# Kernel tuning notes

Measured on AMD Instinct MI355X. Metric: run time of the kernel, lower is better.

Reference implementation:

```python
import jax, jax.numpy as jnp
import numpy as np
from math import sqrt

B, T_IN, N = 32, 12, 512
C = 32                 # d_model (residual == dilation channels)
SKIP_CH, END_CH = 256, 512
OUT_DIM = 12
NHEADS, CH1 = 4, 32    # graph generator heads / per-head dim
L = 8                  # blocks(4) * layers(2)
DILATIONS = [1, 2, 1, 2, 1, 2, 1, 2]
RF = 13                # receptive field = 1 + 4*(2^2 - 1)
KS = [10, 20, 40, 500]
EPS = 1e-5


def conv1x1(x, w, b):
    # x: (B,Cin,N,T), w: (Cout,Cin)
    return jnp.einsum('bcnt,oc->bont', x, w) + b[None, :, None, None]


def dconv(x, w, b, d):
    # dilated temporal conv, kernel (1,2): w (Cout,Cin,2); out T' = T - d
    Tc = x.shape[-1]
    y = (jnp.einsum('bcnt,oc->bont', x[..., :Tc - d], w[:, :, 0])
         + jnp.einsum('bcnt,oc->bont', x[..., d:], w[:, :, 1]))
    return y + b[None, :, None, None]


def gcn_apply(x, A, w, b, batched):
    # x (B,c,N,T); A (S,N,N) static or (B,S,N,N) dynamic; out channels = mlp((S+1)*c)
    Bb, c, n, t = x.shape
    sub = 'bcvt,bsvw->bscwt' if batched else 'bcvt,svw->bscwt'
    x1 = jnp.einsum(sub, x, A).reshape(Bb, -1, n, t)
    return conv1x1(jnp.concatenate([x, x1], axis=1), w, b)


def setup_inputs() -> dict:
    key = jax.random.key(0)
    ks = iter(jax.random.split(key, 64))
    def nrm(shape, fan):
        return jax.random.normal(next(ks), shape, jnp.float32) / np.float32(sqrt(fan))
    inp = {}
    inp['input'] = jax.random.normal(next(ks), (B, T_IN, N), jnp.float32)
    inp['supports'] = jax.random.uniform(next(ks), (2, N, N), jnp.float32) / np.float32(N)
    inp['emb'] = jax.random.normal(next(ks), (1, N, 12), jnp.float32)
    inp['embds_w'] = nrm((12, 1), 12); inp['embds_b'] = jnp.zeros((1,), jnp.float32)
    inp['wl_w'] = nrm((12, CH1 * NHEADS), 12); inp['wl_b'] = jnp.zeros((CH1 * NHEADS,), jnp.float32)
    inp['wr_w'] = nrm((12, CH1 * NHEADS), 12); inp['wr_b'] = jnp.zeros((CH1 * NHEADS,), jnp.float32)
    inp['start_w'] = nrm((C, 1), 1); inp['start_b'] = jnp.zeros((C,), jnp.float32)
    inp['filter_w'] = nrm((L, C, C, 2), 2 * C); inp['filter_b'] = jnp.zeros((L, C), jnp.float32)
    inp['gate_w'] = nrm((L, C, C, 2), 2 * C); inp['gate_b'] = jnp.zeros((L, C), jnp.float32)
    inp['skip_w'] = nrm((L, SKIP_CH, C), C); inp['skip_b'] = jnp.zeros((L, SKIP_CH), jnp.float32)
    inp['bn_g'] = jnp.ones((L, C), jnp.float32); inp['bn_b'] = jnp.zeros((L, C), jnp.float32)
    inp['gconv_w'] = nrm((L, C, 5 * C), 5 * C); inp['gconv_b'] = jnp.zeros((L, C), jnp.float32)
    inp['dyn_w'] = nrm((L, C, 5 * C), 5 * C); inp['dyn_b'] = jnp.zeros((L, C), jnp.float32)
    inp['end1_w'] = nrm((END_CH, SKIP_CH), SKIP_CH); inp['end1_b'] = jnp.zeros((END_CH,), jnp.float32)
    inp['end2_w'] = nrm((OUT_DIM, END_CH), END_CH); inp['end2_b'] = jnp.zeros((OUT_DIM,), jnp.float32)
    return inp


def reference(input, supports, emb, embds_w, embds_b, wl_w, wl_b, wr_w, wr_b,
              start_w, start_b, filter_w, filter_b, gate_w, gate_b,
              skip_w, skip_b, bn_g, bn_b, gconv_w, gconv_b, dyn_w, dyn_b,
              end1_w, end1_b, end2_w, end2_b):
    x_in = jnp.transpose(input, (0, 2, 1))[:, None]           # (B,1,N,12)
    # Embedding: project time dim to 1, add learned node embedding (broadcast back to 12)
    g = (x_in @ embds_w + embds_b) + emb                      # (B,1,N,12)
    feature = g[:, 0]                                         # (B,N,12)
    # multi-head attention scores -> dynamic adjacency candidates
    l = (feature @ wl_w + wl_b).reshape(B, N, NHEADS, CH1).transpose(0, 2, 1, 3)
    r = (feature @ wr_w + wr_b).reshape(B, N, NHEADS, CH1).transpose(0, 2, 1, 3)
    att = jnp.einsum('bhnd,bhmd->bhnm', l, r) / np.float32(sqrt(CH1))   # (B,4,N,N)
    # per-head top-k sparsify (scatter into -1e20) then row softmax
    bi = jnp.arange(B)[:, None, None]
    ri = jnp.arange(N)[None, :, None]
    heads = []
    for h in range(NHEADS):
        a = att[:, h]
        kv, ki = jax.lax.top_k(a, min(KS[h], N))
        m = jnp.full((B, N, N), -1e20, a.dtype).at[bi, ri, ki].set(kv)
        heads.append(jax.nn.softmax(m, axis=-1))
    dyn = jnp.stack(heads, axis=1)                            # (B,4,N,N)
    # static supports: [a0, a0@a0, a1, a1@a1]
    s0, s1 = supports[0], supports[1]
    sup = jnp.stack([s0, s0 @ s0, s1, s1 @ s1], axis=0)        # (4,N,N)
    # left-pad time to receptive field
    x = jnp.pad(x_in, ((0, 0), (0, 0), (0, 0), (RF - T_IN, 0)))
    x = conv1x1(x, start_w, start_b)                          # (B,C,N,13)
    skip = None
    for i, d in enumerate(DILATIONS):
        residual = x
        x = jnp.tanh(dconv(x, filter_w[i], filter_b[i], d)) * jax.nn.sigmoid(dconv(x, gate_w[i], gate_b[i], d))
        s = conv1x1(x, skip_w[i], skip_b[i])
        skip = s if skip is None else s + skip[..., -s.shape[-1]:]
        x = gcn_apply(x, dyn, dyn_w[i], dyn_b[i], True)
        x = gcn_apply(x, sup, gconv_w[i], gconv_b[i], False)
        x = x + residual[..., -x.shape[-1]:]
        # BatchNorm2d in eval mode (running_mean=0, running_var=1)
        x = x / np.float32(sqrt(1.0 + EPS)) * bn_g[i][None, :, None, None] + bn_b[i][None, :, None, None]
    x = jax.nn.relu(skip)                                     # (B,SKIP_CH,N,1)
    x = jax.nn.relu(conv1x1(x, end1_w, end1_b))
    x = conv1x1(x, end2_w, end2_b)                            # (B,12,N,1)
    return x[..., 0]                                          # (B,12,N)
```

## Files before the change

kernel.cpp:

```cpp
#include <hip/hip_runtime.h>
#include <math.h>

#define BB 32
#define NNODE 512
#define TIN 12
#define CCH 32
#define NH 4
#define DDIM 32
#define NL 8
#define SKC 256
#define ENDC 512
#define ODIM 12
#define RFP 13

typedef __attribute__((ext_vector_type(8))) short bf16x8;
typedef __attribute__((ext_vector_type(4))) float f32x4;

__device__ __forceinline__ float sigmoidf_(float x){ return 1.0f/(1.0f+expf(-x)); }
__device__ __forceinline__ unsigned short f2bf(float f){
  unsigned u = __float_as_uint(f);
  u += 0x7FFFu + ((u >> 16) & 1u);
  return (unsigned short)(u >> 16);
}
__device__ __forceinline__ float bf2f(unsigned short h){
  return __uint_as_float(((unsigned)h) << 16);
}
__device__ __forceinline__ void gload16(const void* g, void* l){
  __builtin_amdgcn_global_load_lds(
      (const __attribute__((address_space(1))) void*)g,
      (__attribute__((address_space(3))) void*)l, 16, 0, 0);
}

__global__ void k_feat_lr(const float* __restrict__ input, const float* __restrict__ emb,
                          const float* __restrict__ embds_w, const float* __restrict__ embds_b,
                          const float* __restrict__ wl_w, const float* __restrict__ wl_b,
                          const float* __restrict__ wr_w, const float* __restrict__ wr_b,
                          float* __restrict__ lbuf, float* __restrict__ rbuf){
  int bn = blockIdx.x;
  int b = bn >> 9, n = bn & 511;
  int j = threadIdx.x;
  __shared__ float f[TIN];
  if (j < TIN){
    float s = 0.f;
    for (int t = 0; t < TIN; ++t) s += input[(b*TIN + t)*NNODE + n] * embds_w[t];
    f[j] = s + embds_b[0] + emb[n*TIN + j];
  }
  __syncthreads();
  float lv = wl_b[j], rv = wr_b[j];
  for (int t = 0; t < TIN; ++t){
    float ft = f[t];
    lv += ft * wl_w[t*128 + j];
    rv += ft * wr_w[t*128 + j];
  }
  int h = j >> 5, d = j & 31;
  int o = ((b*NH + h)*NNODE + n)*DDIM + d;
  lbuf[o] = lv; rbuf[o] = rv;
}

__global__ __launch_bounds__(256) void k_att(const float* __restrict__ lbuf,
                      const float* __restrict__ rbuf, float* __restrict__ att){
  int bh = blockIdx.z;
  int n0 = blockIdx.y * 32, m0 = blockIdx.x * 32;
  int tid = threadIdx.x;
  int tx = tid & 31, ty = tid >> 5;
  __shared__ float Ls[32][33], Rs[32][33];
  const float* lb = lbuf + (size_t)bh*NNODE*DDIM;
  const float* rb = rbuf + (size_t)bh*NNODE*DDIM;
  for (int i = tid; i < 1024; i += 256){
    int r = i >> 5, c = i & 31;
    Ls[r][c] = lb[(n0+r)*DDIM + c];
    Rs[r][c] = rb[(m0+r)*DDIM + c];
  }
  __syncthreads();
  float acc[4] = {0.f,0.f,0.f,0.f};
  for (int d = 0; d < 32; ++d){
    float rv = Rs[tx][d];
    #pragma unroll
    for (int j = 0; j < 4; ++j) acc[j] += Ls[ty + 8*j][d] * rv;
  }
  #pragma unroll
  for (int j = 0; j < 4; ++j)
    att[((size_t)bh*NNODE + n0+ty+8*j)*NNODE + m0 + tx] = acc[j] / sqrtf(32.0f);
}

__global__ __launch_bounds__(256) void k_topk_softmax(float* __restrict__ att){
  __shared__ int hist[4*256];
  int tid = threadIdx.x;
  int wid = tid >> 6, lane = tid & 63;
  int row = blockIdx.x*4 + wid;
  int h = (row >> 9) & 3;
  int k = (h==0)?10:(h==1)?20:(h==2)?40:500;
  float* rp = att + (size_t)row * NNODE;
  int* hh = hist + wid*256;
  float v[8]; unsigned a[8];
  #pragma unroll
  for (int j = 0; j < 8; ++j){
    v[j] = rp[j*64 + lane];
    unsigned u = __float_as_uint(v[j]);
    a[j] = (u & 0x80000000u) ? ~u : (u | 0x80000000u);
  }
  float m = v[0];
  #pragma unroll
  for (int j = 1; j < 8; ++j) m = fmaxf(m, v[j]);
  for (int off = 32; off; off >>= 1) m = fmaxf(m, __shfl_down(m, off, 64));
  float mx = __shfl(m, 0, 64);
  unsigned pfx = 0u; int kr = k;
  for (int rnd = 0; rnd < 4; ++rnd){
    int sh = 24 - rnd*8;
    #pragma unroll
    for (int i = 0; i < 4; ++i) hh[lane*4+i] = 0;
    __builtin_amdgcn_wave_barrier();
    #pragma unroll
    for (int j = 0; j < 8; ++j){
      bool c = (rnd == 0) || ((a[j] >> (sh+8)) == (pfx >> (sh+8)));
      if (c) atomicAdd(&hh[(a[j] >> sh) & 255], 1);
    }
    __builtin_amdgcn_wave_barrier();
    asm volatile("s_waitcnt lgkmcnt(0)" ::: "memory");
    int h0 = hh[lane*4], h1 = hh[lane*4+1], h2 = hh[lane*4+2], h3 = hh[lane*4+3];
    int s3 = h3, s2 = h2+s3, s1 = h1+s2, s0 = h0+s1;
    int t = s0;
    #pragma unroll
    for (int off = 1; off < 64; off <<= 1){
      int y = __shfl_down(t, off, 64);
      if (lane + off < 64) t += y;
    }
    int Asuf = __shfl_down(t, 1, 64);
    if (lane == 63) Asuf = 0;
    int cs0 = s0+Asuf, cs1 = s1+Asuf, cs2 = s2+Asuf, cs3 = s3+Asuf;
    int found = 0, dloc = 0, krloc = 0;
    if (cs0 >= kr && cs0-h0 < kr){ found=1; dloc=lane*4+0; krloc = kr-(cs0-h0); }
    if (cs1 >= kr && cs1-h1 < kr){ found=1; dloc=lane*4+1; krloc = kr-(cs1-h1); }
    if (cs2 >= kr && cs2-h2 < kr){ found=1; dloc=lane*4+2; krloc = kr-(cs2-h2); }
    if (cs3 >= kr && cs3-h3 < kr){ found=1; dloc=lane*4+3; krloc = kr-(cs3-h3); }
    unsigned long long msk = __ballot(found);
    int src = __ffsll((unsigned long long)msk) - 1;
    int db = __shfl(dloc, src, 64);
    kr = __shfl(krloc, src, 64);
    pfx = pfx | ((unsigned)db << sh);
  }
  unsigned uth = pfx; int neq = kr;
  unsigned long long em[8];
  #pragma unroll
  for (int j = 0; j < 8; ++j) em[j] = __ballot(a[j] == uth);
  int pcum[8]; int run = 0;
  #pragma unroll
  for (int j = 0; j < 8; ++j){ pcum[j] = run; run += (int)__popcll(em[j]); }
  unsigned long long below = (1ull << lane) - 1ull;
  float e[8]; float ssum = 0.f;
  #pragma unroll
  for (int j = 0; j < 8; ++j){
    bool kp = a[j] > uth;
    if (!kp && a[j] == uth){
      int rank = pcum[j] + (int)__popcll(em[j] & below);
      kp = rank < neq;
    }
    e[j] = kp ? expf(v[j] - mx) : 0.f;
    ssum += e[j];
  }
  for (int off = 32; off; off >>= 1) ssum += __shfl_down(ssum, off, 64);
  float tot = __shfl(ssum, 0, 64);
  unsigned short* rp16 = (unsigned short*)rp;
  #pragma unroll
  for (int j = 0; j < 8; ++j) rp16[j*64 + lane] = f2bf(e[j] / tot);
}

__global__ __launch_bounds__(256) void k_transpose_dyn(const unsigned short* __restrict__ dynBf,
                                                       unsigned short* __restrict__ dynT){
  int bs = blockIdx.z;
  int v0 = blockIdx.x*64, w0 = blockIdx.y*64;
  __shared__ unsigned short Ts[64][66];
  const unsigned short* S = dynBf + (size_t)bs*NNODE*1024;
  unsigned short* D = dynT + (size_t)bs*NNODE*NNODE;
  int tid = threadIdx.x;
  for (int i = tid; i < 4096; i += 256){
    int r = i >> 6, c = i & 63;
    Ts[r][c] = S[(size_t)(v0+r)*1024 + w0 + c];
  }
  __syncthreads();
  for (int i = tid; i < 4096; i += 256){
    int r = i >> 6, c = i & 63;
    D[(size_t)(w0+r)*NNODE + v0 + c] = Ts[c][r];
  }
}

__global__ __launch_bounds__(256) void k_supT_copy(const float* __restrict__ supports,
                                                   unsigned short* __restrict__ supT){
  int w = blockIdx.z;
  int v0 = blockIdx.x*64, n0 = blockIdx.y*64;
  __shared__ float Ts[64][65];
  const float* S = supports + (size_t)w*NNODE*NNODE;
  int tid = threadIdx.x;
  for (int i = tid; i < 4096; i += 256){
    int r = i >> 6, c = i & 63;
    Ts[r][c] = S[(size_t)(v0+r)*NNODE + n0 + c];
  }
  __syncthreads();
  for (int i = tid; i < 4096; i += 256){
    int r = i >> 6, c = i & 63;
    supT[((size_t)(2*w)*NNODE + n0 + r)*NNODE + v0 + c] = f2bf(Ts[c][r]);
  }
}

__global__ __launch_bounds__(256) void k_supT_sq(const float* __restrict__ supports,
                                                 unsigned short* __restrict__ supT){
  int which = blockIdx.z;
  const float* A = supports + (size_t)which*NNODE*NNODE;
  int w0 = blockIdx.x * 32, v0 = blockIdx.y * 32;
  int tid = threadIdx.x;
  int tx = tid & 31, tyg = tid >> 5;
  __shared__ float As[32][33], Bs[32][33], Cs[32][33];
  float acc[4] = {0.f,0.f,0.f,0.f};
  for (int k0 = 0; k0 < NNODE; k0 += 32){
    int lc = tid >> 3, lu0 = (tid & 7) * 4;
    __syncthreads();
    for (int u = 0; u < 4; ++u){
      As[lc][lu0+u] = A[(size_t)(v0+lc)*NNODE + k0 + lu0 + u];
      Bs[lc][lu0+u] = A[(size_t)(k0+lc)*NNODE + w0 + lu0 + u];
    }
    __syncthreads();
    for (int u = 0; u < 32; ++u){
      float bw = Bs[u][tx];
      #pragma unroll
      for (int j = 0; j < 4; ++j) acc[j] += As[tyg + 8*j][u] * bw;
    }
  }
  __syncthreads();
  #pragma unroll
  for (int j = 0; j < 4; ++j) Cs[tyg + 8*j][tx] = acc[j];
  __syncthreads();
  for (int i = tid; i < 1024; i += 256){
    int wl = i >> 5, vl = i & 31;
    supT[((size_t)(2*which+1)*NNODE + w0 + wl)*NNODE + v0 + vl] = f2bf(Cs[vl][wl]);
  }
}

__global__ void k_make_x0(const float* __restrict__ input, const float* __restrict__ start_w,
                          const float* __restrict__ start_b, float* __restrict__ x0){
  int idx = blockIdx.x*256 + threadIdx.x;
  const int total = BB*RFP*CCH*NNODE;
  if (idx >= total) return;
  int n = idx & 511;
  int rest = idx >> 9;
  int c = rest & 31; rest >>= 5;
  int t = rest % RFP;
  int b = rest / RFP;
  float v = (t == 0) ? 0.f : input[((size_t)b*TIN + (t-1))*NNODE + n];
  x0[idx] = start_w[c] * v + start_b[c];
}

__global__ __launch_bounds__(256) void k_dconv_act(const float* __restrict__ x,
      const float* __restrict__ fw, const float* __restrict__ fb,
      const float* __restrict__ gw, const float* __restrict__ gb,
      unsigned short* __restrict__ out,
      const float* __restrict__ sw, const float* __restrict__ sb,
      float* __restrict__ skip,
      int Tin, int Tp, int dil, int skipInit){
  int n0 = blockIdx.x * 64;
  int t = blockIdx.y;
  int b = blockIdx.z;
  int tid = threadIdx.x;
  int lane = tid & 63, cg = tid >> 6;
  __shared__ float X0[32][64], X1[32][64];
  __shared__ float fwl[32][32][2], gwl[32][32][2];
  __shared__ float gs[32][64];
  const float* xb0 = x + ((size_t)(b*Tin + t)*CCH)*NNODE;
  const float* xb1 = x + ((size_t)(b*Tin + t + dil)*CCH)*NNODE;
  for (int i = tid; i < 32*64; i += 256){
    int c = i >> 6, nn2 = i & 63;
    X0[c][nn2] = xb0[c*NNODE + n0 + nn2];
    X1[c][nn2] = xb1[c*NNODE + n0 + nn2];
  }
  for (int i = tid; i < 2048; i += 256){
    ((float*)fwl)[i] = fw[i];
    ((float*)gwl)[i] = gw[i];
  }
  __syncthreads();
  float F[8], G[8];
  #pragma unroll
  for (int j = 0; j < 8; ++j){ int c = cg*8 + j; F[j] = fb[c]; G[j] = gb[c]; }
  for (int cp = 0; cp < 32; ++cp){
    float x0v = X0[cp][lane], x1v = X1[cp][lane];
    #pragma unroll
    for (int j = 0; j < 8; ++j){
      int c = cg*8 + j;
      F[j] += x0v * fwl[c][cp][0] + x1v * fwl[c][cp][1];
      G[j] += x0v * gwl[c][cp][0] + x1v * gwl[c][cp][1];
    }
  }
  unsigned short* ob = out + ((size_t)(b*Tp + t)*CCH)*NNODE;
  #pragma unroll
  for (int j = 0; j < 8; ++j){
    int c = cg*8 + j;
    float gv = tanhf(F[j]) * sigmoidf_(G[j]);
    gs[c][lane] = gv;
    ob[c*NNODE + n0 + lane] = f2bf(gv);
  }
  if (t == Tp - 1){
    __syncthreads();
    float* skb = skip + ((size_t)b*SKC)*NNODE + n0 + lane;
    for (int er = 0; er < 64; ++er){
      int e = cg*64 + er;
      float acc2 = sb[e];
      #pragma unroll
      for (int c = 0; c < 32; ++c) acc2 += sw[e*32 + c] * gs[c][lane];
      float* dst = skb + (size_t)e*NNODE;
      *dst = skipInit ? acc2 : (*dst + acc2);
    }
  }
}

__global__ __launch_bounds__(256) void k_gcn_gemm(
    const unsigned short* __restrict__ A, const unsigned short* __restrict__ BT,
    const float* __restrict__ w, const float* __restrict__ bias,
    unsigned short* __restrict__ outBf, float* __restrict__ outF,
    const float* __restrict__ res, const float* __restrict__ bng,
    const float* __restrict__ bnb, int Tp, int dil, long long bStride){
  __shared__ short smem[16384 + 5376];
  short* AsL = smem;
  short* BsL = smem + 8192;
  short* Wc  = smem + 16384;
  short* Tt  = smem;
  int tid = threadIdx.x;
  int b = blockIdx.z;
  int n032 = blockIdx.x * 32;
  int t0 = blockIdx.y * 4;
  int Mb = Tp * 32;
  int rowBase = b*Mb + blockIdx.y*128;
  const unsigned short* Bb = BT + (size_t)b * bStride;
  int wid = tid >> 6, lane = tid & 63;
  int wm = wid >> 1, wn = wid & 1;
  int l15 = lane & 15, l4 = lane >> 4;
  for (int i = tid; i < 5120; i += 256){
    int o = i / 160, kk = i - o*160;
    Wc[o*168 + kk] = (short)f2bf(w[o*160 + ((kk < 128) ? (32 + kk) : (kk - 128))]);
  }
  f32x4 acc[4][4];
  #pragma unroll
  for (int mf = 0; mf < 4; ++mf)
    #pragma unroll
    for (int nf = 0; nf < 4; ++nf)
      acc[mf][nf] = (f32x4){0.f, 0.f, 0.f, 0.f};
  for (int k0 = 0; k0 < 512; k0 += 64){
    __syncthreads();
    #pragma unroll
    for (int it = 0; it < 4; ++it){
      int r = it*32 + (tid>>3), g = tid & 7;
      gload16(A + (size_t)(rowBase + r)*512 + k0 + ((g ^ (r&7))<<3), AsL + r*64 + (g<<3));
      int s = r >> 5, nl = r & 31;
      gload16(Bb + (size_t)((s<<9) + n032 + nl)*512 + k0 + ((g ^ (r&7))<<3), BsL + r*64 + (g<<3));
    }
    __syncthreads();
    #pragma unroll
    for (int ks = 0; ks < 2; ++ks){
      bf16x8 af[4], bfr[4];
      #pragma unroll
      for (int mf = 0; mf < 4; ++mf){
        int rr = wm*64 + mf*16 + l15;
        af[mf] = *(const bf16x8*)(AsL + rr*64 + (((ks*4 + l4) ^ (rr & 7)) << 3));
      }
      #pragma unroll
      for (int nf = 0; nf < 4; ++nf){
        int rr = wn*64 + nf*16 + l15;
        bfr[nf] = *(const bf16x8*)(BsL + rr*64 + (((ks*4 + l4) ^ (rr & 7)) << 3));
      }
      #pragma unroll
      for (int mf = 0; mf < 4; ++mf)
        #pragma unroll
        for (int nf = 0; nf < 4; ++nf)
          acc[mf][nf] = __builtin_amdgcn_mfma_f32_16x16x32_bf16(af[mf], bfr[nf], acc[mf][nf], 0, 0, 0);
    }
  }
  const float inv = 1.0f / sqrtf(1.0f + 1e-5f);
  for (int t = 0; t < 4; ++t){
    __syncthreads();
    if (wm == (t >> 1)){
      #pragma unroll
      for (int mf2 = 0; mf2 < 2; ++mf2){
        int mf = (t & 1)*2 + mf2;
        #pragma unroll
        for (int nf = 0; nf < 4; ++nf){
          int c128 = wn*64 + nf*16 + l15;
          int s = c128 >> 5, nl = c128 & 31;
          #pragma unroll
          for (int r = 0; r < 4; ++r){
            int cROW = mf2*16 + l4*4 + r;
            Tt[nl*168 + s*32 + cROW] = (short)f2bf(acc[mf][nf][r]);
          }
        }
      }
    }
    for (int i = tid; i < 1024; i += 256){
      int c = i >> 5, nl = i & 31;
      Tt[nl*168 + 128 + c] =
        (short)A[(size_t)(b*Mb + (t0+t)*32 + c)*512 + n032 + nl];
    }
    __syncthreads();
    f32x4 am = (f32x4){0.f,0.f,0.f,0.f};
    #pragma unroll
    for (int ks = 0; ks < 5; ++ks){
      bf16x8 af = *(const bf16x8*)(Wc + (wm*16 + l15)*168 + ks*32 + l4*8);
      bf16x8 bf = *(const bf16x8*)(Tt + (wn*16 + l15)*168 + ks*32 + l4*8);
      am = __builtin_amdgcn_mfma_f32_16x16x32_bf16(af, bf, am, 0, 0, 0);
    }
    if (t0 + t < Tp){
      int btG = b*Tp + t0 + t;
      #pragma unroll
      for (int r = 0; r < 4; ++r){
        int o = wm*16 + l4*4 + r;
        int nl = wn*16 + l15;
        size_t oidx = (size_t)(btG*32 + o)*512 + n032 + nl;
        float val = am[r] + bias[o];
        if (outBf){
          outBf[oidx] = f2bf(val);
        } else {
          float resv = res[(size_t)((b*(Tp+dil) + t0 + t + dil)*32 + o)*512 + n032 + nl];
          outF[oidx] = (val + resv) * (bng[o]*inv) + bnb[o];
        }
      }
    }
  }
}

__global__ __launch_bounds__(256) void k_gemm(
    const unsigned short* __restrict__ A, const unsigned short* __restrict__ BT,
    unsigned short* __restrict__ Y, int Mb, long long bStride,
    int K, int Ystride, int relu){
  __shared__ short As[128][64];
  __shared__ short Bs[128][64];
  int tid = threadIdx.x;
  int n0 = blockIdx.x * 128;
  int rowBase = blockIdx.z * Mb + blockIdx.y * 128;
  int rowEnd  = blockIdx.z * Mb + Mb;
  const unsigned short* Bb = BT + (size_t)blockIdx.z * bStride;
  int wid = tid >> 6, lane = tid & 63;
  int wm = wid >> 1, wn = wid & 1;
  int l15 = lane & 15, l4 = lane >> 4;
  f32x4 acc[4][4];
  #pragma unroll
  for (int mf = 0; mf < 4; ++mf)
    #pragma unroll
    for (int nf = 0; nf < 4; ++nf)
      acc[mf][nf] = (f32x4){0.f, 0.f, 0.f, 0.f};
  for (int k0 = 0; k0 < K; k0 += 64){
    __syncthreads();
    #pragma unroll
    for (int it = 0; it < 4; ++it){
      int r = it*32 + (tid>>3), g = tid & 7;
      gload16(A + (size_t)(rowBase + r)*K + k0 + ((g ^ (r&7))<<3), &As[r][g<<3]);
      gload16(Bb + (size_t)(n0 + r)*K + k0 + ((g ^ (r&7))<<3), &Bs[r][g<<3]);
    }
    __syncthreads();
    #pragma unroll
    for (int ks = 0; ks < 2; ++ks){
      bf16x8 af[4], bfr[4];
      #pragma unroll
      for (int mf = 0; mf < 4; ++mf){
        int r = wm*64 + mf*16 + l15;
        af[mf] = *(const bf16x8*)&As[r][(((ks*4 + l4) ^ (r & 7)) << 3)];
      }
      #pragma unroll
      for (int nf = 0; nf < 4; ++nf){
        int r = wn*64 + nf*16 + l15;
        bfr[nf] = *(const bf16x8*)&Bs[r][(((ks*4 + l4) ^ (r & 7)) << 3)];
      }
      #pragma unroll
      for (int mf = 0; mf < 4; ++mf)
        #pragma unroll
        for (int nf = 0; nf < 4; ++nf)
          acc[mf][nf] = __builtin_amdgcn_mfma_f32_16x16x32_bf16(af[mf], bfr[nf], acc[mf][nf], 0, 0, 0);
    }
  }
  #pragma unroll
  for (int mf = 0; mf < 4; ++mf){
    #pragma unroll
    for (int nf = 0; nf < 4; ++nf){
      #pragma unroll
      for (int r = 0; r < 4; ++r){
        int row = rowBase + wm*64 + mf*16 + l4*4 + r;
        if (row < rowEnd){
          int col = n0 + wn*64 + nf*16 + l15;
          float v = acc[mf][nf][r];
          if (relu) v = v > 0.f ? v : 0.f;
          Y[(size_t)row*Ystride + col] = f2bf(v);
        }
      }
    }
  }
}

__global__ __launch_bounds__(256) void k_skipT(const float* __restrict__ skip,
                                               unsigned short* __restrict__ skT){
  int b = blockIdx.z, e0 = blockIdx.y*64, n0 = blockIdx.x*64;
  __shared__ float Ts[64][65];
  int tid = threadIdx.x;
  for (int i = tid; i < 4096; i += 256){
    int r = i >> 6, c = i & 63;
    Ts[r][c] = skip[((size_t)b*SKC + e0 + r)*NNODE + n0 + c];
  }
  __syncthreads();
  for (int i = tid; i < 4096; i += 256){
    int r = i >> 6, c = i & 63;
    float v = Ts[c][r];
    skT[((size_t)b*NNODE + n0 + r)*SKC + e0 + c] = f2bf(v > 0.f ? v : 0.f);
  }
}

__global__ void k_cvt(const float* __restrict__ src, unsigned short* __restrict__ dst, int n){
  int i = blockIdx.x*256 + threadIdx.x;
  if (i < n) dst[i] = f2bf(src[i]);
}
__global__ void k_cvt_e2(const float* __restrict__ e2w, unsigned short* __restrict__ dst){
  int i = blockIdx.x*256 + threadIdx.x;
  if (i < 16*ENDC){
    int o = i >> 9;
    dst[i] = (o < ODIM) ? f2bf(e2w[(size_t)o*ENDC + (i & 511)]) : (unsigned short)0;
  }
}

__global__ __launch_bounds__(256) void k_end2(const unsigned short* __restrict__ hid,
    const unsigned short* __restrict__ e2wB, const float* __restrict__ e2b,
    float* __restrict__ out){
  int rowBase = blockIdx.x * 64;
  int tid = threadIdx.x;
  int lane = tid & 63, w = tid >> 6;
  int l15 = lane & 15, l4 = lane >> 4;
  __shared__ unsigned short e2s[16][520];
  __shared__ float Cs[16][68];
  for (int i = tid; i < 4096; i += 256){
    int r = i >> 8, c2 = (i & 255) * 2;
    *(unsigned*)&e2s[r][c2] = *(const unsigned*)&e2wB[(size_t)r*ENDC + c2];
  }
  __syncthreads();
  f32x4 acc = (f32x4){0.f,0.f,0.f,0.f};
  const unsigned short* Ab = hid + (size_t)(rowBase + w*16 + l15)*ENDC;
  #pragma unroll
  for (int kk = 0; kk < 16; ++kk){
    bf16x8 af = *(const bf16x8*)(Ab + kk*32 + l4*8);
    bf16x8 bf = *(const bf16x8*)&e2s[l15][kk*32 + l4*8];
    acc = __builtin_amdgcn_mfma_f32_16x16x32_bf16(af, bf, acc, 0, 0, 0);
  }
  #pragma unroll
  for (int r = 0; r < 4; ++r)
    Cs[l15][w*16 + l4*4 + r] = acc[r];
  __syncthreads();
  for (int i = tid; i < ODIM*64; i += 256){
    int o = i >> 6, nl = i & 63;
    int gr = rowBase + nl;
    int b = gr >> 9, n = gr & 511;
    out[((size_t)(b*ODIM + o))*NNODE + n] = Cs[o][nl] + e2b[o];
  }
}

extern "C" void kernel_launch(void* const* d_in, const int* in_sizes, int n_in,
                              void* d_out, int out_size, void* d_ws, size_t ws_size,
                              hipStream_t stream){
  const float* input   = (const float*)d_in[0];
  const float* supports= (const float*)d_in[1];
  const float* emb     = (const float*)d_in[2];
  const float* embds_w = (const float*)d_in[3];
  const float* embds_b = (const float*)d_in[4];
  const float* wl_w    = (const float*)d_in[5];
  const float* wl_b    = (const float*)d_in[6];
  const float* wr_w    = (const float*)d_in[7];
  const float* wr_b    = (const float*)d_in[8];
  const float* start_w = (const float*)d_in[9];
  const float* start_b = (const float*)d_in[10];
  const float* filter_w= (const float*)d_in[11];
  const float* filter_b= (const float*)d_in[12];
  const float* gate_w  = (const float*)d_in[13];
  const float* gate_b  = (const float*)d_in[14];
  const float* skip_w  = (const float*)d_in[15];
  const float* skip_b  = (const float*)d_in[16];
  const float* bn_g    = (const float*)d_in[17];
  const float* bn_b    = (const float*)d_in[18];
  const float* gconv_w = (const float*)d_in[19];
  const float* gconv_b = (const float*)d_in[20];
  const float* dyn_w   = (const float*)d_in[21];
  const float* dyn_b   = (const float*)d_in[22];
  const float* end1_w  = (const float*)d_in[23];
  const float* end1_b  = (const float*)d_in[24];
  const float* end2_w  = (const float*)d_in[25];
  const float* end2_b  = (const float*)d_in[26];
  float* out = (float*)d_out;

  float* ws = (float*)d_ws;
  float* dyn = ws;
  unsigned short* act = (unsigned short*)ws;
  float* bufP = ws + 3145728;
  float* bufQ = ws + 3145728 + 6815744;
  float* skip = ws + 16777216;
  unsigned short* R = (unsigned short*)(ws + 20971520);
  unsigned short* dynT = (unsigned short*)(ws + 33554432);
  float* lbuf = ws + 33554432;
  float* rbuf = ws + 33554432 + 2097152;
  unsigned short* supT = (unsigned short*)(ws + 33554432 + 16777216);
  unsigned short* skT  = (unsigned short*)(ws + 50855936);
  unsigned short* hid  = (unsigned short*)(ws + 52953088);
  unsigned short* e1wB = (unsigned short*)(ws + 57147392);
  unsigned short* e2wB = (unsigned short*)(ws + 57212928);

  hipLaunchKernelGGL(k_feat_lr, dim3(BB*NNODE), dim3(128), 0, stream,
                     input, emb, embds_w, embds_b, wl_w, wl_b, wr_w, wr_b, lbuf, rbuf);
  hipLaunchKernelGGL(k_att, dim3(16, 16, BB*NH), dim3(256), 0, stream, lbuf, rbuf, dyn);
  hipLaunchKernelGGL(k_topk_softmax, dim3(BB*NH*NNODE/4), dim3(256), 0, stream, dyn);
  hipLaunchKernelGGL(k_transpose_dyn, dim3(8, 8, BB*NH), dim3(256), 0, stream,
                     (const unsigned short*)dyn, dynT);
  hipLaunchKernelGGL(k_supT_copy, dim3(8, 8, 2), dim3(256), 0, stream, supports, supT);
  hipLaunchKernelGGL(k_supT_sq, dim3(16, 16, 2), dim3(256), 0, stream, supports, supT);
  {
    int total = BB*RFP*CCH*NNODE;
    hipLaunchKernelGGL(k_make_x0, dim3((total+255)/256), dim3(256), 0, stream,
                       input, start_w, start_b, bufP);
  }

  const int dil_[8] = {1,2,1,2,1,2,1,2};
  int T = RFP;
  float* P = bufP; float* Q = bufQ;
  for (int i = 0; i < NL; ++i){
    int d = dil_[i], Tp = T - d;
    int mT = (Tp*32 + 127)/128;
    hipLaunchKernelGGL(k_dconv_act, dim3(8, Tp, BB), dim3(256), 0, stream,
        P, filter_w + i*2048, filter_b + i*32, gate_w + i*2048, gate_b + i*32,
        act, skip_w + i*SKC*CCH, skip_b + i*SKC, skip, T, Tp, d, (i==0)?1:0);
    hipLaunchKernelGGL(k_gcn_gemm, dim3(16, mT, BB), dim3(256), 0, stream,
        act, dynT, dyn_w + i*5120, dyn_b + i*32,
        R, (float*)nullptr, (const float*)nullptr, (const float*)nullptr,
        (const float*)nullptr, Tp, d, (long long)NH*NNODE*NNODE);
    hipLaunchKernelGGL(k_gcn_gemm, dim3(16, mT, BB), dim3(256), 0, stream,
        R, supT, gconv_w + i*5120, gconv_b + i*32,
        (unsigned short*)nullptr, Q, P, bn_g + i*32, bn_b + i*32, Tp, d, 0LL);
    float* tmp = P; P = Q; Q = tmp;
    T = Tp;
  }
  hipLaunchKernelGGL(k_skipT, dim3(8, 4, BB), dim3(256), 0, stream, skip, skT);
  hipLaunchKernelGGL(k_cvt, dim3((ENDC*SKC+255)/256), dim3(256), 0, stream,
                     end1_w, e1wB, ENDC*SKC);
  hipLaunchKernelGGL(k_cvt_e2, dim3((16*ENDC+255)/256), dim3(256), 0, stream,
                     end2_w, e2wB);
  hipLaunchKernelGGL(k_gemm, dim3(4, 128, 1), dim3(256), 0, stream,
      skT, e1wB, hid, BB*NNODE, 0LL, 256, 512, 1);
  hipLaunchKernelGGL(k_end2, dim3(256), dim3(256), 0, stream, hid, e2wB, end1_b, out);
}
```

Before: 1.799 ms.

## Split skip accumulation out of dconv kernel and drop its LDS staging

After: 4.875 ms. +170.9%, slower.

```diff
diff --git a/kernel.cpp b/kernel.cpp
--- a/kernel.cpp
+++ b/kernel.cpp
@@ -252,61 +252,67 @@
 __global__ __launch_bounds__(256) void k_dconv_act(const float* __restrict__ x,
       const float* __restrict__ fw, const float* __restrict__ fb,
       const float* __restrict__ gw, const float* __restrict__ gb,
-      unsigned short* __restrict__ out,
-      const float* __restrict__ sw, const float* __restrict__ sb,
-      float* __restrict__ skip,
-      int Tin, int Tp, int dil, int skipInit){
+      unsigned short* __restrict__ out, int Tin, int Tp, int dil){
   int n0 = blockIdx.x * 64;
   int t = blockIdx.y;
   int b = blockIdx.z;
   int tid = threadIdx.x;
   int lane = tid & 63, cg = tid >> 6;
-  __shared__ float X0[32][64], X1[32][64];
-  __shared__ float fwl[32][32][2], gwl[32][32][2];
-  __shared__ float gs[32][64];
-  const float* xb0 = x + ((size_t)(b*Tin + t)*CCH)*NNODE;
-  const float* xb1 = x + ((size_t)(b*Tin + t + dil)*CCH)*NNODE;
-  for (int i = tid; i < 32*64; i += 256){
-    int c = i >> 6, nn2 = i & 63;
-    X0[c][nn2] = xb0[c*NNODE + n0 + nn2];
-    X1[c][nn2] = xb1[c*NNODE + n0 + nn2];
-  }
-  for (int i = tid; i < 2048; i += 256){
-    ((float*)fwl)[i] = fw[i];
-    ((float*)gwl)[i] = gw[i];
-  }
-  __syncthreads();
+  int n = n0 + lane;
+  const float* xb0 = x + ((size_t)(b*Tin + t)*CCH)*NNODE + n;
+  const float* xb1 = xb0 + (size_t)dil*CCH*NNODE;
+  float x0[32], x1[32];
+  #pragma unroll
+  for (int c = 0; c < 32; ++c){ x0[c] = xb0[c*NNODE]; x1[c] = xb1[c*NNODE]; }
   float F[8], G[8];
   #pragma unroll
   for (int j = 0; j < 8; ++j){ int c = cg*8 + j; F[j] = fb[c]; G[j] = gb[c]; }
+  #pragma unroll
   for (int cp = 0; cp < 32; ++cp){
-    float x0v = X0[cp][lane], x1v = X1[cp][lane];
+    float a = x0[cp], bv = x1[cp];
     #pragma unroll
     for (int j = 0; j < 8; ++j){
       int c = cg*8 + j;
-      F[j] += x0v * fwl[c][cp][0] + x1v * fwl[c][cp][1];
-      G[j] += x0v * gwl[c][cp][0] + x1v * gwl[c][cp][1];
-    }
-  }
-  unsigned short* ob = out + ((size_t)(b*Tp + t)*CCH)*NNODE;
+      F[j] += a * fw[c*64 + cp*2] + bv * fw[c*64 + cp*2 + 1];
+      G[j] += a * gw[c*64 + cp*2] + bv * gw[c*64 + cp*2 + 1];
+    }
+  }
+  unsigned short* ob = out + ((size_t)(b*Tp + t)*CCH)*NNODE + n;
   #pragma unroll
   for (int j = 0; j < 8; ++j){
     int c = cg*8 + j;
-    float gv = tanhf(F[j]) * sigmoidf_(G[j]);
-    gs[c][lane] = gv;
-    ob[c*NNODE + n0 + lane] = f2bf(gv);
-  }
-  if (t == Tp - 1){
-    __syncthreads();
-    float* skb = skip + ((size_t)b*SKC)*NNODE + n0 + lane;
-    for (int er = 0; er < 64; ++er){
-      int e = cg*64 + er;
-      float acc2 = sb[e];
-      #pragma unroll
-      for (int c = 0; c < 32; ++c) acc2 += sw[e*32 + c] * gs[c][lane];
-      float* dst = skb + (size_t)e*NNODE;
-      *dst = skipInit ? acc2 : (*dst + acc2);
-    }
+    ob[c*NNODE] = f2bf(tanhf(F[j]) * sigmoidf_(G[j]));
+  }
+}
+
+__global__ __launch_bounds__(256) void k_skip_accum(const unsigned short* __restrict__ act,
+     const float* __restrict__ sw, const float* __restrict__ sb,
+     float* __restrict__ skip, int Tp, int init){
+  int n0 = blockIdx.x * 64;
+  int e0 = blockIdx.y * 32;
+  int b = blockIdx.z;
+  int tid = threadIdx.x;
+  int lane = tid & 63, eg = tid >> 6;
+  __shared__ float Xs[32][64];
+  const unsigned short* ab = act + ((size_t)(b*Tp + Tp-1)*CCH)*NNODE;
+  for (int i = tid; i < 2048; i += 256){
+    int c = i >> 6, nn2 = i & 63;
+    Xs[c][nn2] = bf2f(ab[c*NNODE + n0 + nn2]);
+  }
+  __syncthreads();
+  float acc[8];
+  #pragma unroll
+  for (int j = 0; j < 8; ++j) acc[j] = sb[e0 + eg*8 + j];
+  for (int c = 0; c < 32; ++c){
+    float xv = Xs[c][lane];
+    #pragma unroll
+    for (int j = 0; j < 8; ++j) acc[j] += sw[(e0 + eg*8 + j)*CCH + c] * xv;
+  }
+  #pragma unroll
+  for (int j = 0; j < 8; ++j){
+    int e = e0 + eg*8 + j;
+    float* dst = &skip[((size_t)b*SKC + e)*NNODE + n0 + lane];
+    *dst = init ? acc[j] : (*dst + acc[j]);
   }
 }
 
@@ -622,7 +628,9 @@
     int mT = (Tp*32 + 127)/128;
     hipLaunchKernelGGL(k_dconv_act, dim3(8, Tp, BB), dim3(256), 0, stream,
         P, filter_w + i*2048, filter_b + i*32, gate_w + i*2048, gate_b + i*32,
-        act, skip_w + i*SKC*CCH, skip_b + i*SKC, skip, T, Tp, d, (i==0)?1:0);
+        act, T, Tp, d);
+    hipLaunchKernelGGL(k_skip_accum, dim3(8, 8, BB), dim3(256), 0, stream,
+        act, skip_w + i*SKC*CCH, skip_b + i*SKC, skip, Tp, (i==0)?1:0);
     hipLaunchKernelGGL(k_gcn_gemm, dim3(16, mT, BB), dim3(256), 0, stream,
         act, dynT, dyn_w + i*5120, dyn_b + i*32,
         R, (float*)nullptr, (const float*)nullptr, (const float*)nullptr,
```
